# Optimization experiments

Measured on AMD Instinct MI355X. Metric: run time of the kernel, lower is better.

Reference implementation:

```python
import jax, jax.numpy as jnp
import numpy as np
from jax.scipy.ndimage import map_coordinates

N, H, W = 64, 1024, 1024

def setup_inputs() -> dict:
    key = jax.random.key(0)
    k1, k2, k3 = jax.random.split(key, 3)
    inputs = jax.random.normal(k1, (1, N, H, W, 1), dtype=jnp.float32)
    flux = jax.random.normal(k2, (N, 1, 1, 1), dtype=jnp.float32) * 0.05  # tf.random_normal_initializer stddev
    noise = jnp.zeros((N, 1, 1, 1), dtype=jnp.float32)
    dydx = jax.random.normal(k3, (N, 2), dtype=jnp.float32)  # sub-pixel shifts
    return {"inputs": inputs, "flux": flux, "noise": noise, "dydx": dydx}

def reference(inputs, flux, noise, dydx):
    # inputs: [1, N, H, W, 1]; per-frame bilinear shift (scipy order=1, mode='mirror'),
    # then elementwise flux scale + noise bias.
    x = inputs[0, ..., 0]  # [N, H, W]
    yy = jnp.arange(H, dtype=jnp.float32)[:, None]  # [H,1]
    xx = jnp.arange(W, dtype=jnp.float32)[None, :]  # [1,W]

    def shift_one(img, s):
        # scipy.ndimage.shift: output[i,j] = input[i - dy, j - dx], bilinear, mirror boundary
        cy = jnp.broadcast_to(yy - s[0], (H, W))
        cx = jnp.broadcast_to(xx - s[1], (H, W))
        return map_coordinates(img, [cy, cx], order=1, mode='mirror')

    shifted = jax.vmap(shift_one)(x, dydx)  # [N, H, W]
    shifted = shifted.reshape(inputs.shape)  # [1, N, H, W, 1]
    return shifted * flux + noise
```

## Files before the change

kernel.cpp:

```cpp
#include <hip/hip_runtime.h>

#define NFRAMES 64
#define HH 1024
#define WW 1024
#define QPF_SHIFT 18
#define QPF_MASK  ((1 << QPF_SHIFT) - 1)
#define W4_SHIFT  8
#define W4_MASK   255

__device__ __forceinline__ int mirror_fix(int idx, int s, int m) {
    int t = (idx + s) % m;
    if (t < 0) t += m;
    t -= s;
    return t < 0 ? -t : t;
}

__global__ __launch_bounds__(256) void
flux_shift_kernel(const float* __restrict__ in,
                  const float* __restrict__ flux,
                  const float* __restrict__ noise,
                  const float* __restrict__ dydx,
                  float* __restrict__ out,
                  int total_quads) {
    const int stride = gridDim.x * blockDim.x;
    for (int q = blockIdx.x * blockDim.x + threadIdx.x; q < total_quads; q += stride) {
        const int n   = q >> QPF_SHIFT;
        const int rem = q & QPF_MASK;
        const int y   = rem >> W4_SHIFT;
        const int x   = (rem & W4_MASK) << 2;

        const float dy = dydx[2 * n];
        const float dx = dydx[2 * n + 1];
        const float fl = flux[n];
        const float bi = noise[n];

        const float nky = floorf(-dy);
        const float nkx = floorf(-dx);
        const float fy = -dy - nky;
        const float fx = -dx - nkx;
        const int ky = (int)nky;
        const int kx = (int)nkx;

        const int ry0 = y + ky;
        const int cx0 = x + kx;

        const float* __restrict__ base = in + (size_t)n * (HH * WW);
        const float gy = 1.0f - fy;
        const float gx = 1.0f - fx;

        float4 o;
        if ((unsigned)ry0 <= (unsigned)(HH - 2) && (unsigned)cx0 <= (unsigned)(WW - 5)) {
            const float* __restrict__ r0 = base + (size_t)ry0 * WW + cx0;
            const float* __restrict__ r1 = r0 + WW;
            const float a0 = r0[0], a1 = r0[1], a2 = r0[2], a3 = r0[3], a4 = r0[4];
            const float b0 = r1[0], b1 = r1[1], b2 = r1[2], b3 = r1[3], b4 = r1[4];
            const float t0 = gy * a0 + fy * b0;
            const float t1 = gy * a1 + fy * b1;
            const float t2 = gy * a2 + fy * b2;
            const float t3 = gy * a3 + fy * b3;
            const float t4 = gy * a4 + fy * b4;
            o.x = (gx * t0 + fx * t1) * fl + bi;
            o.y = (gx * t1 + fx * t2) * fl + bi;
            o.z = (gx * t2 + fx * t3) * fl + bi;
            o.w = (gx * t3 + fx * t4) * fl + bi;
        } else {
            const int sh = HH - 1, mh = 2 * sh;
            const int sw = WW - 1, mw = 2 * sw;
            const int iy0 = mirror_fix(ry0,     sh, mh);
            const int iy1 = mirror_fix(ry0 + 1, sh, mh);
            const float* __restrict__ r0 = base + (size_t)iy0 * WW;
            const float* __restrict__ r1 = base + (size_t)iy1 * WW;
            float res[4];
            #pragma unroll
            for (int j = 0; j < 4; ++j) {
                const int c0 = mirror_fix(cx0 + j,     sw, mw);
                const int c1 = mirror_fix(cx0 + j + 1, sw, mw);
                const float t0 = gy * r0[c0] + fy * r1[c0];
                const float t1 = gy * r0[c1] + fy * r1[c1];
                res[j] = (gx * t0 + fx * t1) * fl + bi;
            }
            o = make_float4(res[0], res[1], res[2], res[3]);
        }
        *reinterpret_cast<float4*>(out + (size_t)q * 4) = o;
    }
}

extern "C" void kernel_launch(void* const* d_in, const int* in_sizes, int n_in,
                              void* d_out, int out_size, void* d_ws, size_t ws_size,
                              hipStream_t stream) {
    const float* in    = (const float*)d_in[0];
    const float* flux  = (const float*)d_in[1];
    const float* noise = (const float*)d_in[2];
    const float* dydx  = (const float*)d_in[3];
    float* out = (float*)d_out;

    const int total_quads = NFRAMES * HH * (WW / 4);
    const int block = 256;
    const int grid  = 2048;

    flux_shift_kernel<<<grid, block, 0, stream>>>(in, flux, noise, dydx, out, total_quads);
}
```

Baseline: 461.6 us.

## Compute 4x4 output patch per thread with aligned float4 loads of 5 rows

Each thread now produces a 4x4 output tile instead of a 1x4 quad. It loads 5 input rows as aligned float4 pairs and selects the sub-element offset through a templated switch, so vertically adjacent rows are reused in registers rather than reloaded. The grid-stride loop is replaced by one block per (frame, 4-row band). This cuts scalar unaligned loads and redundant row reads, at the cost of higher register use and a divergent switch on the horizontal offset.

```diff
diff --git a/kernel.cpp b/kernel.cpp
--- a/kernel.cpp
+++ b/kernel.cpp
@@ -3,10 +3,6 @@
 #define NFRAMES 64
 #define HH 1024
 #define WW 1024
-#define QPF_SHIFT 18
-#define QPF_MASK  ((1 << QPF_SHIFT) - 1)
-#define W4_SHIFT  8
-#define W4_MASK   255
 
 __device__ __forceinline__ int mirror_fix(int idx, int s, int m) {
     int t = (idx + s) % m;
@@ -15,59 +11,89 @@
     return t < 0 ? -t : t;
 }
 
+template<int O>
+__device__ __forceinline__ void compute_patch(const float4 (&L)[5][2],
+                                              float fy, float gy,
+                                              float fx, float gx,
+                                              float fl, float bi,
+                                              float4 (&res)[4]) {
+    float w[5][5];
+    #pragma unroll
+    for (int r = 0; r < 5; ++r) {
+        const float* f = reinterpret_cast<const float*>(&L[r][0]);
+        #pragma unroll
+        for (int c = 0; c < 5; ++c) w[r][c] = f[O + c];
+    }
+    #pragma unroll
+    for (int r = 0; r < 4; ++r) {
+        float t[5];
+        #pragma unroll
+        for (int c = 0; c < 5; ++c) t[c] = gy * w[r][c] + fy * w[r + 1][c];
+        res[r].x = (gx * t[0] + fx * t[1]) * fl + bi;
+        res[r].y = (gx * t[1] + fx * t[2]) * fl + bi;
+        res[r].z = (gx * t[2] + fx * t[3]) * fl + bi;
+        res[r].w = (gx * t[3] + fx * t[4]) * fl + bi;
+    }
+}
+
 __global__ __launch_bounds__(256) void
 flux_shift_kernel(const float* __restrict__ in,
                   const float* __restrict__ flux,
                   const float* __restrict__ noise,
                   const float* __restrict__ dydx,
-                  float* __restrict__ out,
-                  int total_quads) {
-    const int stride = gridDim.x * blockDim.x;
-    for (int q = blockIdx.x * blockDim.x + threadIdx.x; q < total_quads; q += stride) {
-        const int n   = q >> QPF_SHIFT;
-        const int rem = q & QPF_MASK;
-        const int y   = rem >> W4_SHIFT;
-        const int x   = (rem & W4_MASK) << 2;
+                  float* __restrict__ out) {
+    const int band = blockIdx.x & 255;
+    const int n    = blockIdx.x >> 8;
+    const int y0   = band << 2;
+    const int x    = threadIdx.x << 2;
 
-        const float dy = dydx[2 * n];
-        const float dx = dydx[2 * n + 1];
-        const float fl = flux[n];
-        const float bi = noise[n];
+    const float dy = dydx[2 * n];
+    const float dx = dydx[2 * n + 1];
+    const float fl = flux[n];
+    const float bi = noise[n];
 
-        const float nky = floorf(-dy);
-        const float nkx = floorf(-dx);
-        const float fy = -dy - nky;
-        const float fx = -dx - nkx;
-        const int ky = (int)nky;
-        const int kx = (int)nkx;
+    const float nky = floorf(-dy);
+    const float nkx = floorf(-dx);
+    const float fy = -dy - nky;
+    const float fx = -dx - nkx;
+    const int ky = (int)nky;
+    const int kx = (int)nkx;
+    const float gy = 1.0f - fy;
+    const float gx = 1.0f - fx;
 
-        const int ry0 = y + ky;
+    const int ry = y0 + ky;
+    const int o  = kx & 3;
+    const int A  = x + kx - o;
+
+    const float* __restrict__ base = in + (size_t)n * (HH * WW);
+    float* __restrict__ ob = out + (size_t)n * (HH * WW) + (size_t)y0 * WW + x;
+
+    if (ry >= 0 && ry + 4 <= HH - 1 && A >= 0 && A <= WW - 8) {
+        const float* __restrict__ p = base + (size_t)ry * WW + A;
+        float4 L[5][2];
+        #pragma unroll
+        for (int r = 0; r < 5; ++r) {
+            L[r][0] = *reinterpret_cast<const float4*>(p + (size_t)r * WW);
+            L[r][1] = *reinterpret_cast<const float4*>(p + (size_t)r * WW + 4);
+        }
+        float4 res[4];
+        switch (o) {
+            case 0:  compute_patch<0>(L, fy, gy, fx, gx, fl, bi, res); break;
+            case 1:  compute_patch<1>(L, fy, gy, fx, gx, fl, bi, res); break;
+            case 2:  compute_patch<2>(L, fy, gy, fx, gx, fl, bi, res); break;
+            default: compute_patch<3>(L, fy, gy, fx, gx, fl, bi, res); break;
+        }
+        #pragma unroll
+        for (int r = 0; r < 4; ++r)
+            *reinterpret_cast<float4*>(ob + (size_t)r * WW) = res[r];
+    } else {
+        const int sh = HH - 1, mh = 2 * sh;
+        const int sw = WW - 1, mw = 2 * sw;
         const int cx0 = x + kx;
-
-        const float* __restrict__ base = in + (size_t)n * (HH * WW);
-        const float gy = 1.0f - fy;
-        const float gx = 1.0f - fx;
-
-        float4 o;
-        if ((unsigned)ry0 <= (unsigned)(HH - 2) && (unsigned)cx0 <= (unsigned)(WW - 5)) {
-            const float* __restrict__ r0 = base + (size_t)ry0 * WW + cx0;
-            const float* __restrict__ r1 = r0 + WW;
-            const float a0 = r0[0], a1 = r0[1], a2 = r0[2], a3 = r0[3], a4 = r0[4];
-            const float b0 = r1[0], b1 = r1[1], b2 = r1[2], b3 = r1[3], b4 = r1[4];
-            const float t0 = gy * a0 + fy * b0;
-            const float t1 = gy * a1 + fy * b1;
-            const float t2 = gy * a2 + fy * b2;
-            const float t3 = gy * a3 + fy * b3;
-            const float t4 = gy * a4 + fy * b4;
-            o.x = (gx * t0 + fx * t1) * fl + bi;
-            o.y = (gx * t1 + fx * t2) * fl + bi;
-            o.z = (gx * t2 + fx * t3) * fl + bi;
-            o.w = (gx * t3 + fx * t4) * fl + bi;
-        } else {
-            const int sh = HH - 1, mh = 2 * sh;
-            const int sw = WW - 1, mw = 2 * sw;
-            const int iy0 = mirror_fix(ry0,     sh, mh);
-            const int iy1 = mirror_fix(ry0 + 1, sh, mh);
+        #pragma unroll
+        for (int r = 0; r < 4; ++r) {
+            const int iy0 = mirror_fix(y0 + r + ky,     sh, mh);
+            const int iy1 = mirror_fix(y0 + r + ky + 1, sh, mh);
             const float* __restrict__ r0 = base + (size_t)iy0 * WW;
             const float* __restrict__ r1 = base + (size_t)iy1 * WW;
             float res[4];
@@ -79,9 +105,9 @@
                 const float t1 = gy * r0[c1] + fy * r1[c1];
                 res[j] = (gx * t0 + fx * t1) * fl + bi;
             }
-            o = make_float4(res[0], res[1], res[2], res[3]);
+            *reinterpret_cast<float4*>(ob + (size_t)r * WW) =
+                make_float4(res[0], res[1], res[2], res[3]);
         }
-        *reinterpret_cast<float4*>(out + (size_t)q * 4) = o;
     }
 }
 
@@ -94,9 +120,8 @@
     const float* dydx  = (const float*)d_in[3];
     float* out = (float*)d_out;
 
-    const int total_quads = NFRAMES * HH * (WW / 4);
+    const int grid  = NFRAMES * (HH / 4);
     const int block = 256;
-    const int grid  = 2048;
 
-    flux_shift_kernel<<<grid, block, 0, stream>>>(in, flux, noise, dydx, out, total_quads);
+    flux_shift_kernel<<<grid, block, 0, stream>>>(in, flux, noise, dydx, out);
 }
```

Result: faster. 441.0 us (-4.5%).
